# Kernel tuning notes

Measured on AMD Instinct MI355X. Metric: run time of the kernel, lower is better.

## Reference

```python
import jax, jax.numpy as jnp
import numpy as np

D = 1024
LD = 64
NTR = 8192
NT = 8192
DY = 128

def setup_inputs() -> dict:
    key = jax.random.key(0)
    k1, k2, k3, k4 = jax.random.split(key, 4)
    xtr = jax.random.normal(k1, (NTR, D), dtype=jnp.float32)
    ytr = jax.random.normal(k2, (NTR, DY), dtype=jnp.float32)
    xt = jax.random.normal(k3, (NT, D), dtype=jnp.float32)
    A = jax.random.normal(k4, (D, LD), dtype=jnp.float32) / (D ** 0.5)
    return {"xtr": xtr, "ytr": ytr, "xt": xt, "A": A}

def reference(xtr, ytr, xt, A):
    # mean-center both train and test features with the train mean
    mu = jnp.mean(xtr, axis=0, keepdims=True)          # [1, d]
    qtr = (xtr - mu) @ A                                # [Ntr, ld]
    qt = (xt - mu) @ A                                  # [Nt, ld]
    scores = jnp.einsum('nl,ml->nm', qt, qtr)           # [Nt, Ntr]
    E = jax.nn.softmax(scores, axis=1)                  # row-wise softmax over train points
    return E @ ytr                                      # [Nt, dy]
```

## Files before the change

### kernel.cpp

```cpp
#include <hip/hip_runtime.h>
#include <hip/hip_bf16.h>

#define D    1024
#define LD   64
#define NTR  8192
#define NT   8192
#define DY   128

#define SHIFT 40.0f
#define NCHUNK 16
#define CHUNK (NTR / NCHUNK)

typedef __attribute__((ext_vector_type(8))) short bf16x8;
typedef __attribute__((ext_vector_type(8))) _Float16 half8;
typedef __attribute__((ext_vector_type(4))) short short4_;
typedef __attribute__((ext_vector_type(4))) float f4;

static __device__ __forceinline__ short f2bf(float f) {
    __hip_bfloat16 h = __float2bfloat16(f);
    short s; __builtin_memcpy(&s, &h, 2); return s;
}
static __device__ __forceinline__ float bf2f(short s) {
    __hip_bfloat16 h; __builtin_memcpy(&h, &s, 2); return __bfloat162float(h);
}
static __device__ __forceinline__ short f2h(float f) {
    _Float16 h = (_Float16)f;
    short s; __builtin_memcpy(&s, &h, 2); return s;
}
static __device__ __forceinline__ float h2f(short s) {
    _Float16 h; __builtin_memcpy(&h, &s, 2); return (float)h;
}

static __device__ __forceinline__ void gload_lds16(const void* g, void* l) {
    __builtin_amdgcn_global_load_lds(
        (const __attribute__((address_space(1))) unsigned int*)g,
        (__attribute__((address_space(3))) unsigned int*)l,
        16, 0, 0);
}

#define WAIT_VM8() __builtin_amdgcn_s_waitcnt(0x3F78)

__global__ __launch_bounds__(256) void proj_prep(const float* __restrict__ xt,
                                                 const float* __restrict__ xtr,
                                                 const float* __restrict__ A,
                                                 const float* __restrict__ ytr,
                                                 short* __restrict__ qt_hi,
                                                 short* __restrict__ qt_lo,
                                                 short* __restrict__ ktr,
                                                 float* __restrict__ muAp,
                                                 short* __restrict__ vtile) {
    __shared__ __align__(16) float xbuf[4][3][1024];

    int tid = threadIdx.x;
    int b = blockIdx.x;

    if (b >= 256) {
        __shared__ float tile[64][66];
        int bz = b - 256;
        int t0 = (bz & 127) * 64;
        int d0 = (bz >> 7) * 64;
        int c = tid & 63;
        int r4 = tid >> 6;
        #pragma unroll
        for (int i = 0; i < 16; ++i) {
            int r = i * 4 + r4;
            tile[r][c] = ytr[(long)(t0 + r) * DY + d0 + c];
        }
        __syncthreads();
        #pragma unroll
        for (int i = 0; i < 16; ++i) {
            int r = i * 4 + r4;
            int t = t0 + c;
            int dy = d0 + r;
            long idx = (long)(t >> 5) * 4096 + (long)dy * 32
                     + ((((t >> 3) & 3) ^ (dy & 3)) << 3) + (t & 7);
            vtile[idx] = f2bf(tile[c][r]);
        }
        return;
    }

    int wave = tid >> 6;
    int lane = tid & 63;
    int quad = lane >> 4;
    int l16 = lane & 15;

    int g = b * 4 + wave;
    bool is_test = g < (NT / 16);
    int row0 = (is_test ? g : g - NT / 16) * 16;
    const float* x = is_test ? xt : xtr;

    int sr = lane >> 4;
    int cg0 = (lane & 15);

    f4 acc[4];
    #pragma unroll
    for (int ct = 0; ct < 4; ++ct) acc[ct] = (f4){0.f, 0.f, 0.f, 0.f};

    int pr0 = ((quad * 2) ^ (l16 & 7)) * 4;
    int pr1 = (((quad * 2) | 1) ^ (l16 & 7)) * 4;

#define PROJ_DMA(S, BUF)                                                        \
    {                                                                           \
        int kk0 = ((S) & 15) * 64;                                              \
        _Pragma("unroll")                                                       \
        for (int j = 0; j < 4; ++j) {                                           \
            int r = j * 4 + sr;                                                 \
            int cgl = cg0 ^ (r & 7);                                            \
            gload_lds16(x + (long)(row0 + r) * D + kk0 + cgl * 4,               \
                        &xbuf[wave][BUF][j * 256]);                             \
        }                                                                       \
    }

    PROJ_DMA(0, 0)
    PROJ_DMA(1, 1)

    #pragma unroll 1
    for (int s = 0; s < 16; ++s) {
        int cur = s % 3;
        PROJ_DMA(s + 2, (s + 2) % 3)
        WAIT_VM8();

        const float* xrow = &xbuf[wave][cur][l16 * 64];
        bf16x8 ah[2], al[2];
        #pragma unroll
        for (int h = 0; h < 2; ++h) {
            f4 v0 = *(const f4*)(xrow + h * 32 + pr0);
            f4 v1 = *(const f4*)(xrow + h * 32 + pr1);
            #pragma unroll
            for (int e = 0; e < 4; ++e) {
                short hi0 = f2bf(v0[e]);
                short hi1 = f2bf(v1[e]);
                ah[h][e]     = hi0;
                ah[h][e + 4] = hi1;
                al[h][e]     = f2bf(v0[e] - bf2f(hi0));
                al[h][e + 4] = f2bf(v1[e] - bf2f(hi1));
            }
        }

        int k0 = s * 64;
        #pragma unroll
        for (int ct = 0; ct < 4; ++ct) {
            const float* Acol = A + ct * 16 + l16;
            bf16x8 bh0, bh1, bl0, bl1;
            #pragma unroll
            for (int j = 0; j < 8; ++j) {
                float a0 = Acol[(long)(k0 + quad * 8 + j) * LD];
                float a1 = Acol[(long)(k0 + 32 + quad * 8 + j) * LD];
                short h0 = f2bf(a0);
                short h1 = f2bf(a1);
                bh0[j] = h0; bl0[j] = f2bf(a0 - bf2f(h0));
                bh1[j] = h1; bl1[j] = f2bf(a1 - bf2f(h1));
            }
            f4 a = acc[ct];
            a = __builtin_amdgcn_mfma_f32_16x16x32_bf16(ah[0], bh0, a, 0, 0, 0);
            a = __builtin_amdgcn_mfma_f32_16x16x32_bf16(al[0], bh0, a, 0, 0, 0);
            a = __builtin_amdgcn_mfma_f32_16x16x32_bf16(ah[0], bl0, a, 0, 0, 0);
            a = __builtin_amdgcn_mfma_f32_16x16x32_bf16(ah[1], bh1, a, 0, 0, 0);
            a = __builtin_amdgcn_mfma_f32_16x16x32_bf16(al[1], bh1, a, 0, 0, 0);
            a = __builtin_amdgcn_mfma_f32_16x16x32_bf16(ah[1], bl1, a, 0, 0, 0);
            acc[ct] = a;
        }
    }
#undef PROJ_DMA

    #pragma unroll
    for (int ct = 0; ct < 4; ++ct) {
        int col = ct * 16 + l16;
        #pragma unroll
        for (int r = 0; r < 4; ++r) {
            int grow = row0 + quad * 4 + r;
            float qv = acc[ct][r];
            if (is_test) {
                short hi = f2h(qv);
                qt_hi[(long)grow * LD + col] = hi;
                qt_lo[(long)grow * LD + col] = f2h(qv - h2f(hi));
            } else {
                int tl = grow & 31;
                long idx = (long)(grow >> 5) * 2048 + tl * 64
                         + ((((col >> 3) ^ (tl & 7))) << 3) + (col & 7);
                ktr[idx] = f2h(qv);
            }
        }
        if (!is_test) {
            float s = acc[ct][0] + acc[ct][1] + acc[ct][2] + acc[ct][3];
            s += __shfl_xor(s, 16);
            s += __shfl_xor(s, 32);
            if (quad == 0) muAp[(long)(g - NT / 16) * 64 + col] = s;
        }
    }
}

__global__ __launch_bounds__(256) void c_kernel(const short* __restrict__ ktr,
                                                const float* __restrict__ muAp,
                                                float* __restrict__ cc) {
    __shared__ float red[4][64];
    __shared__ __align__(16) float muAs[64];
    int l = threadIdx.x & 63;
    int g = threadIdx.x >> 6;
    float ms = 0.f;
    #pragma unroll 8
    for (int p = g; p < 512; p += 4) ms += muAp[(long)p * 64 + l];
    red[g][l] = ms;
    __syncthreads();
    if (threadIdx.x < 64)
        muAs[l] = (red[0][l] + red[1][l] + red[2][l] + red[3][l]) *
                  (1.0f / (float)NTR);
    __syncthreads();

    int t = blockIdx.x * 256 + threadIdx.x;
    int tl = t & 31;
    long rb = (long)(t >> 5) * 2048 + tl * 64;
    float s = SHIFT;
    #pragma unroll
    for (int c = 0; c < 8; ++c) {
        int pos = (c ^ (tl & 7)) << 3;
        bf16x8 h8 = *(const bf16x8*)&ktr[rb + pos];
        f4 m0 = *(const f4*)&muAs[c * 8];
        f4 m1 = *(const f4*)&muAs[c * 8 + 4];
        #pragma unroll
        for (int j = 0; j < 4; ++j) {
            s += h2f(h8[j]) * m0[j];
            s += h2f(h8[j + 4]) * m1[j];
        }
    }
    cc[t] = s;
}

__global__ __launch_bounds__(256, 3) void flash_kernel(const short* __restrict__ qt_hi,
                                                       const short* __restrict__ qt_lo,
                                                       const short* __restrict__ ksw,
                                                       const short* __restrict__ vtile,
                                                       const float* __restrict__ cc,
                                                       short* __restrict__ Opart,
                                                       float* __restrict__ Lpart) {
    __shared__ __align__(16) short kbh[2][2048];
    __shared__ __align__(16) short vbuf[2][4096];
    __shared__ __align__(16) short ptile[4][1280];

    int tid = threadIdx.x;
    int wave = tid >> 6;
    int lane = tid & 63;
    int quad = lane >> 4;
    int l16 = lane & 15;

    int kc = blockIdx.x & 15;
    int qi = blockIdx.x >> 4;
    int q0w = qi * 128 + wave * 32;
    int tile0 = kc * 16;
    int kc0 = kc * CHUNK;

    int soff = wave * 512 + lane * 8;
    int ldso = wave * 512;

    half8 qh[2][2], ql[2][2];
    #pragma unroll
    for (int rt = 0; rt < 2; ++rt) {
        const short* qrh = qt_hi + (long)(q0w + rt * 16 + l16) * LD + quad * 8;
        const short* qrl = qt_lo + (long)(q0w + rt * 16 + l16) * LD + quad * 8;
        qh[rt][0] = *(const half8*)qrh;
        qh[rt][1] = *(const half8*)(qrh + 32);
        ql[rt][0] = *(const half8*)qrl;
        ql[rt][1] = *(const half8*)(qrl + 32);
    }

    bf16x8 onef;
    #pragma unroll
    for (int i = 0; i < 8; ++i) onef[i] = (short)0x3F80;

    f4 Ov[2][8];
    f4 Lv[2];
    #pragma unroll
    for (int rt = 0; rt < 2; ++rt) {
        Lv[rt] = (f4){0.f, 0.f, 0.f, 0.f};
        #pragma unroll
        for (int jt = 0; jt < 8; ++jt) Ov[rt][jt] = (f4){0.f, 0.f, 0.f, 0.f};
    }

    short* myp = &ptile[wave][0];
    const int p0 = ((quad ^ (l16 & 7)) << 3);
    const int pv = ((quad ^ (l16 & 3)) << 3);

    gload_lds16(ksw + (long)tile0 * 2048 + soff, &kbh[0][ldso]);
    gload_lds16(vtile + (long)tile0 * 4096 + soff, &vbuf[0][ldso]);
    gload_lds16(vtile + (long)tile0 * 4096 + 2048 + soff, &vbuf[0][2048 + ldso]);
    __syncthreads();

    #pragma unroll 1
    for (int it = 0; it < 16; ++it) {
        int cur = it & 1;

        f4 cv[2];
        #pragma unroll
        for (int tt = 0; tt < 2; ++tt)
            cv[tt] = *(const f4*)&cc[kc0 + it * 32 + tt * 16 + quad * 4];

        if (it < 15) {
            int nb = cur ^ 1;
            long tb = (long)(tile0 + it + 1);
            gload_lds16(ksw + tb * 2048 + soff, &kbh[nb][ldso]);
            gload_lds16(vtile + tb * 4096 + soff, &vbuf[nb][ldso]);
            gload_lds16(vtile + tb * 4096 + 2048 + soff, &vbuf[nb][2048 + ldso]);
        }

        half8 kh[2][2];
        #pragma unroll
        for (int tt = 0; tt < 2; ++tt) {
            int rb = (tt * 16 + l16) * 64;
            kh[tt][0] = *(const half8*)&kbh[cur][rb + p0];
            kh[tt][1] = *(const half8*)&kbh[cur][rb + (p0 ^ 32)];
        }

        f4 s[2][2];
        #pragma unroll
        for (int rt = 0; rt < 2; ++rt) {
            #pragma unroll
            for (int tt = 0; tt < 2; ++tt) {
                f4 a = (f4){0.f, 0.f, 0.f, 0.f};
                a = __builtin_amdgcn_mfma_f32_16x16x32_f16(kh[tt][0], qh[rt][0], a, 0, 0, 0);
                a = __builtin_amdgcn_mfma_f32_16x16x32_f16(kh[tt][0], ql[rt][0], a, 0, 0, 0);
                a = __builtin_amdgcn_mfma_f32_16x16x32_f16(kh[tt][1], qh[rt][1], a, 0, 0, 0);
                a = __builtin_amdgcn_mfma_f32_16x16x32_f16(kh[tt][1], ql[rt][1], a, 0, 0, 0);
                s[rt][tt] = a;
            }
        }

        #pragma unroll
        for (int rt = 0; rt < 2; ++rt) {
            #pragma unroll
            for (int tt = 0; tt < 2; ++tt) {
                short4_ p4;
                p4[0] = f2bf(__expf(s[rt][tt][0] - cv[tt][0]));
                p4[1] = f2bf(__expf(s[rt][tt][1] - cv[tt][1]));
                p4[2] = f2bf(__expf(s[rt][tt][2] - cv[tt][2]));
                p4[3] = f2bf(__expf(s[rt][tt][3] - cv[tt][3]));
                *(short4_*)&myp[(rt * 16 + l16) * 40 + tt * 16 + quad * 4] = p4;
            }
        }

        bf16x8 vf[8];
        #pragma unroll
        for (int jt = 0; jt < 8; ++jt)
            vf[jt] = *(const bf16x8*)&vbuf[cur][(jt * 16 + l16) * 32 + pv];
        #pragma unroll
        for (int rt = 0; rt < 2; ++rt) {
            bf16x8 pf = *(const bf16x8*)&myp[(rt * 16 + l16) * 40 + quad * 8];
            #pragma unroll
            for (int jt = 0; jt < 8; ++jt)
                Ov[rt][jt] = __builtin_amdgcn_mfma_f32_16x16x32_bf16(pf, vf[jt], Ov[rt][jt], 0, 0, 0);
            Lv[rt] = __builtin_amdgcn_mfma_f32_16x16x32_bf16(pf, onef, Lv[rt], 0, 0, 0);
        }

        __syncthreads();
    }

    long ob = (long)kc * NT;
    #pragma unroll
    for (int rt = 0; rt < 2; ++rt) {
        #pragma unroll
        for (int jt = 0; jt < 8; ++jt) {
            #pragma unroll
            for (int r = 0; r < 4; ++r)
                Opart[(ob + q0w + rt * 16 + quad * 4 + r) * DY + jt * 16 + l16] =
                    f2bf(Ov[rt][jt][r]);
        }
        if (l16 == 0) {
            #pragma unroll
            for (int r = 0; r < 4; ++r)
                Lpart[ob + q0w + rt * 16 + quad * 4 + r] = Lv[rt][r];
        }
    }
}

__global__ __launch_bounds__(256) void finalize_kernel(const short* __restrict__ Opart,
                                                       const float* __restrict__ Lpart,
                                                       float* __restrict__ out) {
    long i = ((long)blockIdx.x * 256 + threadIdx.x) * 8;
    long row = i >> 7;
    float L = 0.f;
    f4 a = (f4){0.f, 0.f, 0.f, 0.f};
    f4 b = (f4){0.f, 0.f, 0.f, 0.f};
    #pragma unroll
    for (int kc = 0; kc < NCHUNK; ++kc) {
        L += Lpart[(long)kc * NT + row];
        bf16x8 o = *(const bf16x8*)&Opart[(long)kc * NT * DY + i];
        #pragma unroll
        for (int j = 0; j < 4; ++j) {
            a[j] += bf2f(o[j]);
            b[j] += bf2f(o[j + 4]);
        }
    }
    float linv = 1.0f / L;
    a *= linv; b *= linv;
    *(f4*)&out[i] = a;
    *(f4*)&out[i + 4] = b;
}

extern "C" void kernel_launch(void* const* d_in, const int* in_sizes, int n_in,
                              void* d_out, int out_size, void* d_ws, size_t ws_size,
                              hipStream_t stream) {
    const float* xtr = (const float*)d_in[0];
    const float* ytr = (const float*)d_in[1];
    const float* xt  = (const float*)d_in[2];
    const float* A   = (const float*)d_in[3];
    float* out = (float*)d_out;

    char* w = (char*)d_ws;
    float* muAp  = (float*)w; w += (size_t)512 * 64 * 4;
    float* cc    = (float*)w; w += (size_t)NTR * 4;
    float* Lpart = (float*)w; w += (size_t)NCHUNK * NT * 4;
    short* Opart = (short*)w; w += (size_t)NCHUNK * NT * DY * 2;
    short* qt_hi  = (short*)w; w += (size_t)NT * LD * 2;
    short* qt_lo  = (short*)w; w += (size_t)NT * LD * 2;
    short* ksw    = (short*)w; w += (size_t)NTR * LD * 2;
    short* vtile  = (short*)w; w += (size_t)DY * NTR * 2;
    (void)ws_size; (void)in_sizes; (void)n_in; (void)out_size;

    proj_prep<<<512, 256, 0, stream>>>(xt, xtr, A, ytr,
                                       qt_hi, qt_lo, ksw, muAp, vtile);
    c_kernel<<<32, 256, 0, stream>>>(ksw, muAp, cc);
    flash_kernel<<<1024, 256, 0, stream>>>(qt_hi, qt_lo, ksw, vtile, cc,
                                           Opart, Lpart);
    finalize_kernel<<<(NT * DY) / (256 * 8), 256, 0, stream>>>(Opart, Lpart, out);
}
```

Measured before the change: 173.8 us.

## Center queries up front and double query rows per wave in flash kernel

The per-train-point correction vector cc (k·muA + shift) is replaced by a small kernel that subtracts muA from the stored test projections in place, re-splitting them into hi/lo fp16 halves. This removes the per-iteration cc loads and the c_kernel launch. Each wave now handles 64 query rows instead of 32, so every K/V tile staged in LDS is reused by twice as many queries. The grid halves to 512 blocks and occupancy drops to 2 blocks per CU. The exchange is higher register pressure from 128 accumulator values and fewer waves to hide latency.

```diff
diff --git a/kernel.cpp b/kernel.cpp
--- a/kernel.cpp
+++ b/kernel.cpp
@@ -190,9 +190,9 @@
     }
 }
 
-__global__ __launch_bounds__(256) void c_kernel(const short* __restrict__ ktr,
-                                                const float* __restrict__ muAp,
-                                                float* __restrict__ cc) {
+__global__ __launch_bounds__(256) void center_q(short* __restrict__ qt_hi,
+                                                short* __restrict__ qt_lo,
+                                                const float* __restrict__ muAp) {
     __shared__ float red[4][64];
     __shared__ __align__(16) float muAs[64];
     int l = threadIdx.x & 63;
@@ -207,35 +207,36 @@
                   (1.0f / (float)NTR);
     __syncthreads();
 
-    int t = blockIdx.x * 256 + threadIdx.x;
-    int tl = t & 31;
-    long rb = (long)(t >> 5) * 2048 + tl * 64;
-    float s = SHIFT;
-    #pragma unroll
-    for (int c = 0; c < 8; ++c) {
-        int pos = (c ^ (tl & 7)) << 3;
-        bf16x8 h8 = *(const bf16x8*)&ktr[rb + pos];
-        f4 m0 = *(const f4*)&muAs[c * 8];
-        f4 m1 = *(const f4*)&muAs[c * 8 + 4];
-        #pragma unroll
-        for (int j = 0; j < 4; ++j) {
-            s += h2f(h8[j]) * m0[j];
-            s += h2f(h8[j + 4]) * m1[j];
-        }
-    }
-    cc[t] = s;
-}
-
-__global__ __launch_bounds__(256, 3) void flash_kernel(const short* __restrict__ qt_hi,
+    int t = threadIdx.x;
+    int row = t >> 1;
+    int ch = (t & 1) * 32;
+    long off = (long)blockIdx.x * 128 * LD + (long)row * LD + ch;
+    #pragma unroll
+    for (int c = 0; c < 4; ++c) {
+        bf16x8 hi8 = *(const bf16x8*)&qt_hi[off + c * 8];
+        bf16x8 lo8 = *(const bf16x8*)&qt_lo[off + c * 8];
+        bf16x8 nh, nl;
+        #pragma unroll
+        for (int e = 0; e < 8; ++e) {
+            float q = h2f(hi8[e]) + h2f(lo8[e]) - muAs[ch + c * 8 + e];
+            short hh = f2h(q);
+            nh[e] = hh;
+            nl[e] = f2h(q - h2f(hh));
+        }
+        *(bf16x8*)&qt_hi[off + c * 8] = nh;
+        *(bf16x8*)&qt_lo[off + c * 8] = nl;
+    }
+}
+
+__global__ __launch_bounds__(256, 2) void flash_kernel(const short* __restrict__ qt_hi,
                                                        const short* __restrict__ qt_lo,
                                                        const short* __restrict__ ksw,
                                                        const short* __restrict__ vtile,
-                                                       const float* __restrict__ cc,
                                                        short* __restrict__ Opart,
                                                        float* __restrict__ Lpart) {
     __shared__ __align__(16) short kbh[2][2048];
     __shared__ __align__(16) short vbuf[2][4096];
-    __shared__ __align__(16) short ptile[4][1280];
+    __shared__ __align__(16) short ptile[4][2560];
 
     int tid = threadIdx.x;
     int wave = tid >> 6;
@@ -245,16 +246,15 @@
 
     int kc = blockIdx.x & 15;
     int qi = blockIdx.x >> 4;
-    int q0w = qi * 128 + wave * 32;
+    int q0w = qi * 256 + wave * 64;
     int tile0 = kc * 16;
-    int kc0 = kc * CHUNK;
 
     int soff = wave * 512 + lane * 8;
     int ldso = wave * 512;
 
-    half8 qh[2][2], ql[2][2];
-    #pragma unroll
-    for (int rt = 0; rt < 2; ++rt) {
+    half8 qh[4][2], ql[4][2];
+    #pragma unroll
+    for (int rt = 0; rt < 4; ++rt) {
         const short* qrh = qt_hi + (long)(q0w + rt * 16 + l16) * LD + quad * 8;
         const short* qrl = qt_lo + (long)(q0w + rt * 16 + l16) * LD + quad * 8;
         qh[rt][0] = *(const half8*)qrh;
@@ -267,10 +267,10 @@
     #pragma unroll
     for (int i = 0; i < 8; ++i) onef[i] = (short)0x3F80;
 
-    f4 Ov[2][8];
-    f4 Lv[2];
-    #pragma unroll
-    for (int rt = 0; rt < 2; ++rt) {
+    f4 Ov[4][8];
+    f4 Lv[4];
+    #pragma unroll
+    for (int rt = 0; rt < 4; ++rt) {
         Lv[rt] = (f4){0.f, 0.f, 0.f, 0.f};
         #pragma unroll
         for (int jt = 0; jt < 8; ++jt) Ov[rt][jt] = (f4){0.f, 0.f, 0.f, 0.f};
@@ -288,11 +288,6 @@
     #pragma unroll 1
     for (int it = 0; it < 16; ++it) {
         int cur = it & 1;
-
-        f4 cv[2];
-        #pragma unroll
-        for (int tt = 0; tt < 2; ++tt)
-            cv[tt] = *(const f4*)&cc[kc0 + it * 32 + tt * 16 + quad * 4];
 
         if (it < 15) {
             int nb = cur ^ 1;
@@ -310,9 +305,8 @@
             kh[tt][1] = *(const half8*)&kbh[cur][rb + (p0 ^ 32)];
         }
 
-        f4 s[2][2];
-        #pragma unroll
-        for (int rt = 0; rt < 2; ++rt) {
+        #pragma unroll
+        for (int rt = 0; rt < 4; ++rt) {
             #pragma unroll
             for (int tt = 0; tt < 2; ++tt) {
                 f4 a = (f4){0.f, 0.f, 0.f, 0.f};
@@ -320,42 +314,36 @@
                 a = __builtin_amdgcn_mfma_f32_16x16x32_f16(kh[tt][0], ql[rt][0], a, 0, 0, 0);
                 a = __builtin_amdgcn_mfma_f32_16x16x32_f16(kh[tt][1], qh[rt][1], a, 0, 0, 0);
                 a = __builtin_amdgcn_mfma_f32_16x16x32_f16(kh[tt][1], ql[rt][1], a, 0, 0, 0);
-                s[rt][tt] = a;
-            }
-        }
-
-        #pragma unroll
-        for (int rt = 0; rt < 2; ++rt) {
-            #pragma unroll
-            for (int tt = 0; tt < 2; ++tt) {
                 short4_ p4;
-                p4[0] = f2bf(__expf(s[rt][tt][0] - cv[tt][0]));
-                p4[1] = f2bf(__expf(s[rt][tt][1] - cv[tt][1]));
-                p4[2] = f2bf(__expf(s[rt][tt][2] - cv[tt][2]));
-                p4[3] = f2bf(__expf(s[rt][tt][3] - cv[tt][3]));
+                p4[0] = f2bf(__expf(a[0] - SHIFT));
+                p4[1] = f2bf(__expf(a[1] - SHIFT));
+                p4[2] = f2bf(__expf(a[2] - SHIFT));
+                p4[3] = f2bf(__expf(a[3] - SHIFT));
                 *(short4_*)&myp[(rt * 16 + l16) * 40 + tt * 16 + quad * 4] = p4;
             }
         }
 
-        bf16x8 vf[8];
-        #pragma unroll
-        for (int jt = 0; jt < 8; ++jt)
-            vf[jt] = *(const bf16x8*)&vbuf[cur][(jt * 16 + l16) * 32 + pv];
-        #pragma unroll
-        for (int rt = 0; rt < 2; ++rt) {
-            bf16x8 pf = *(const bf16x8*)&myp[(rt * 16 + l16) * 40 + quad * 8];
-            #pragma unroll
-            for (int jt = 0; jt < 8; ++jt)
-                Ov[rt][jt] = __builtin_amdgcn_mfma_f32_16x16x32_bf16(pf, vf[jt], Ov[rt][jt], 0, 0, 0);
-            Lv[rt] = __builtin_amdgcn_mfma_f32_16x16x32_bf16(pf, onef, Lv[rt], 0, 0, 0);
-        }
+        bf16x8 pf[4];
+        #pragma unroll
+        for (int rt = 0; rt < 4; ++rt)
+            pf[rt] = *(const bf16x8*)&myp[(rt * 16 + l16) * 40 + quad * 8];
+        #pragma unroll
+        for (int jt = 0; jt < 8; ++jt) {
+            bf16x8 vf = *(const bf16x8*)&vbuf[cur][(jt * 16 + l16) * 32 + pv];
+            #pragma unroll
+            for (int rt = 0; rt < 4; ++rt)
+                Ov[rt][jt] = __builtin_amdgcn_mfma_f32_16x16x32_bf16(pf[rt], vf, Ov[rt][jt], 0, 0, 0);
+        }
+        #pragma unroll
+        for (int rt = 0; rt < 4; ++rt)
+            Lv[rt] = __builtin_amdgcn_mfma_f32_16x16x32_bf16(pf[rt], onef, Lv[rt], 0, 0, 0);
 
         __syncthreads();
     }
 
     long ob = (long)kc * NT;
     #pragma unroll
-    for (int rt = 0; rt < 2; ++rt) {
+    for (int rt = 0; rt < 4; ++rt) {
         #pragma unroll
         for (int jt = 0; jt < 8; ++jt) {
             #pragma unroll
@@ -406,7 +394,6 @@
 
     char* w = (char*)d_ws;
     float* muAp  = (float*)w; w += (size_t)512 * 64 * 4;
-    float* cc    = (float*)w; w += (size_t)NTR * 4;
     float* Lpart = (float*)w; w += (size_t)NCHUNK * NT * 4;
     short* Opart = (short*)w; w += (size_t)NCHUNK * NT * DY * 2;
     short* qt_hi  = (short*)w; w += (size_t)NT * LD * 2;
@@ -417,8 +404,8 @@
 
     proj_prep<<<512, 256, 0, stream>>>(xt, xtr, A, ytr,
                                        qt_hi, qt_lo, ksw, muAp, vtile);
-    c_kernel<<<32, 256, 0, stream>>>(ksw, muAp, cc);
-    flash_kernel<<<1024, 256, 0, stream>>>(qt_hi, qt_lo, ksw, vtile, cc,
-                                           Opart, Lpart);
+    center_q<<<64, 256, 0, stream>>>(qt_hi, qt_lo, muAp);
+    flash_kernel<<<512, 256, 0, stream>>>(qt_hi, qt_lo, ksw, vtile,
+                                          Opart, Lpart);
     finalize_kernel<<<(NT * DY) / (256 * 8), 256, 0, stream>>>(Opart, Lpart, out);
 }
```

Result: no change. 172.2 us (-0.9%).
